# Kernel optimization log

Measured on AMD Instinct MI355X. Metric: run time of the kernel, lower is better.

The kernel has to match this reference:

```python
import jax, jax.numpy as jnp
import numpy as np

N = 50000
E = 800000
H = 128

def _mlp_params(key, sizes, biases):
    # sizes: list of (in, out); biases: list of bool
    params = []
    for i, ((fi, fo), b) in enumerate(zip(sizes, biases)):
        k = jax.random.fold_in(key, i)
        bound = 1.0 / np.sqrt(fi)
        W = jax.random.uniform(k, (fi, fo), minval=-bound, maxval=bound, dtype=jnp.float32)
        if b:
            bb = jax.random.uniform(jax.random.fold_in(k, 7), (fo,), minval=-bound, maxval=bound, dtype=jnp.float32)
        else:
            bb = None
        params.append((W, bb))
    return params

def setup_inputs() -> dict:
    key = jax.random.key(0)
    ks = jax.random.split(key, 8)
    h = jax.random.normal(ks[0], (N, H), dtype=jnp.float32)
    pos = jax.random.normal(ks[1], (N, 3), dtype=jnp.float32)
    edge_index = jax.random.randint(ks[2], (2, E), 0, N, dtype=jnp.int32)
    edge_p = _mlp_params(ks[3], [(2 * H + 1, H), (H, H)], [True, True])
    node_p = _mlp_params(ks[4], [(2 * H, H), (H, H)], [True, True])
    coord_p = _mlp_params(ks[5], [(H, H), (H, 1)], [True, False])
    return {
        'h': h, 'pos': pos, 'edge_index': edge_index,
        'eW0': edge_p[0][0], 'eb0': edge_p[0][1], 'eW1': edge_p[1][0], 'eb1': edge_p[1][1],
        'nW0': node_p[0][0], 'nb0': node_p[0][1], 'nW1': node_p[1][0], 'nb1': node_p[1][1],
        'cW0': coord_p[0][0], 'cb0': coord_p[0][1], 'cW1': coord_p[1][0],
    }

def reference(h, pos, edge_index, eW0, eb0, eW1, eb1, nW0, nb0, nW1, nb1, cW0, cb0, cW1):
    row, col = edge_index[0], edge_index[1]
    coord_diff = pos[row] - pos[col]                         # [E, 3]
    radial = jnp.sum(coord_diff ** 2, axis=1, keepdims=True)  # [E, 1]
    edge_feat = jnp.concatenate([h[row], h[col], radial], axis=1)  # [E, 2H+1]
    # edge MLP: Linear -> SiLU -> Linear -> SiLU
    m_ij = jax.nn.silu(edge_feat @ eW0 + eb0)
    m_ij = jax.nn.silu(m_ij @ eW1 + eb1)                     # [E, H]
    # coord MLP: Linear -> SiLU -> Linear(no bias)
    coord_weight = jax.nn.silu(m_ij @ cW0 + cb0) @ cW1       # [E, 1]
    norm = jnp.sqrt(radial + 1e-8)
    coord_update = coord_diff / norm * coord_weight          # [E, 3]
    # scatter-add messages to target nodes
    m_i = jax.ops.segment_sum(m_ij, row, num_segments=h.shape[0])
    node_in = jnp.concatenate([h, m_i], axis=1)              # [N, 2H]
    h_new = h + jax.nn.silu(node_in @ nW0 + nb0) @ nW1 + nb1
    pos_update = jax.ops.segment_sum(coord_update, row, num_segments=pos.shape[0])
    deg = jax.ops.segment_sum(jnp.ones((row.shape[0],), jnp.float32), row, num_segments=pos.shape[0])
    pos_new = pos + pos_update / (deg[:, None] + 1e-6)
    return h_new, pos_new
```

## Files before the change

### kernel.cpp

```cpp
#include <hip/hip_runtime.h>
#include <hip/hip_bf16.h>
#include <cstddef>

#define N_NODES 50000
#define N_EDGES 800000
#define HDIM    128
#define TME     64
#define TMN     64

#define RB128   272
#define RB256   528

#define SCHUNK  512
#define SNBLK   ((N_NODES + SCHUNK - 1) / SCHUNK)

typedef __attribute__((ext_vector_type(4))) float f32x4;
typedef __attribute__((ext_vector_type(8))) short bf16x8;

#define OFF_EW0T 0
#define OFF_EW0B 16384
#define OFF_EW1  32768
#define OFF_CW0  49152
#define OFF_NW0  65536
#define OFF_NW1  98304
#define PACK_ELEMS 114688

__device__ __forceinline__ float silu(float x) {
    float e = __expf(-x);
    return __fdividef(x, 1.0f + e);
}
__device__ __forceinline__ unsigned short f2bf(float f) {
    union { __hip_bfloat16 h; unsigned short u; } cv;
    cv.h = __float2bfloat16(f);
    return cv.u;
}
__device__ __forceinline__ unsigned int f2bf2(float a, float b) {
    union { __hip_bfloat162 h; unsigned int u; } cv;
    cv.h = __float22bfloat162_rn(float2{a, b});
    return cv.u;
}
__device__ __forceinline__ float bf2f(unsigned short u) {
    return __uint_as_float(((unsigned int)u) << 16);
}
__device__ __forceinline__ float bflo(unsigned int u) {
    return __uint_as_float(u << 16);
}
__device__ __forceinline__ float bfhi(unsigned int u) {
    return __uint_as_float(u & 0xffff0000u);
}

__global__ void pack_weights(const float* __restrict__ eW0, const float* __restrict__ eW1,
                             const float* __restrict__ cW0, const float* __restrict__ nW0,
                             const float* __restrict__ nW1, unsigned short* __restrict__ pack)
{
    int g = blockIdx.x * blockDim.x + threadIdx.x;
    int f = g >> 6;
    int lane = g & 63;
    const float* W; int base; int rowoff = 0;
    if (f < 32)       { W = eW0; base = OFF_EW0T; }
    else if (f < 64)  { W = eW0; base = OFF_EW0B; f -= 32; rowoff = 128; }
    else if (f < 96)  { W = eW1; base = OFF_EW1;  f -= 64; }
    else if (f < 128) { W = cW0; base = OFF_CW0;  f -= 96; }
    else if (f < 192) { W = nW0; base = OFF_NW0;  f -= 128; }
    else              { W = nW1; base = OFF_NW1;  f -= 192; }
    int KS = (base == OFF_NW0) ? 8 : 4;
    int cb = f / KS, ks = f % KS;
    int col = cb * 16 + (lane & 15);
    int kbase = rowoff + ks * 32 + ((lane >> 4) << 3);
#pragma unroll
    for (int j = 0; j < 8; ++j)
        pack[(size_t)base + ((size_t)(f * 64 + lane) * 8 + j)] =
            f2bf(W[(size_t)(kbase + j) * HDIM + col]);
}

__global__ __launch_bounds__(256)
void scanA_kernel(const int* __restrict__ cnt, int* __restrict__ bsum) {
    __shared__ int part[256];
    const int b = blockIdx.x, t = threadIdx.x;
    int i0 = b * SCHUNK + t * 2;
    int s = 0;
    if (i0 < N_NODES)     s += cnt[i0];
    if (i0 + 1 < N_NODES) s += cnt[i0 + 1];
    part[t] = s;
    __syncthreads();
    for (int off = 128; off > 0; off >>= 1) {
        if (t < off) part[t] += part[t + off];
        __syncthreads();
    }
    if (t == 0) bsum[b] = part[0];
}

__global__ __launch_bounds__(128)
void scanB_kernel(const int* __restrict__ bsum, int* __restrict__ boff,
                  int* __restrict__ row_start) {
    __shared__ int part[128];
    const int t = threadIdx.x;
    int s = (t < SNBLK) ? bsum[t] : 0;
    part[t] = s;
    __syncthreads();
    for (int off = 1; off < 128; off <<= 1) {
        int tmp = (t >= off) ? part[t - off] : 0;
        __syncthreads();
        part[t] += tmp;
        __syncthreads();
    }
    boff[t] = part[t] - s;
    if (t == 127) row_start[N_NODES] = part[127];
}

__global__ __launch_bounds__(256)
void scanC_kernel(const int* __restrict__ cnt, const int* __restrict__ boff,
                  int* __restrict__ row_start, int* __restrict__ cursor) {
    __shared__ int part[256];
    const int b = blockIdx.x, t = threadIdx.x;
    int i0 = b * SCHUNK + t * 2;
    int c0 = (i0 < N_NODES) ? cnt[i0] : 0;
    int c1 = (i0 + 1 < N_NODES) ? cnt[i0 + 1] : 0;
    int s = c0 + c1;
    part[t] = s;
    __syncthreads();
    for (int off = 1; off < 256; off <<= 1) {
        int tmp = (t >= off) ? part[t - off] : 0;
        __syncthreads();
        part[t] += tmp;
        __syncthreads();
    }
    int base = boff[b] + part[t] - s;
    if (i0 < N_NODES)     { row_start[i0] = base;          cursor[i0] = base; }
    if (i0 + 1 < N_NODES) { row_start[i0 + 1] = base + c0; cursor[i0 + 1] = base + c0; }
}

__global__ void scatter_kernel(const int* __restrict__ eidx, int* __restrict__ cursor,
                               int2* __restrict__ rc) {
    int e = (blockIdx.x * blockDim.x + threadIdx.x) * 4;
    if (e + 3 < N_EDGES) {
        int4 r4 = *(const int4*)(eidx + e);
        int4 c4 = *(const int4*)(eidx + N_EDGES + e);
        int p;
        p = atomicAdd(&cursor[r4.x], 1); rc[p] = int2{r4.x, c4.x};
        p = atomicAdd(&cursor[r4.y], 1); rc[p] = int2{r4.y, c4.y};
        p = atomicAdd(&cursor[r4.z], 1); rc[p] = int2{r4.z, c4.z};
        p = atomicAdd(&cursor[r4.w], 1); rc[p] = int2{r4.w, c4.w};
    } else {
        for (int i = e; i < N_EDGES; ++i) {
            int r = eidx[i], c = eidx[N_EDGES + i];
            int p = atomicAdd(&cursor[r], 1);
            rc[p] = int2{r, c};
        }
    }
}

template<int KS, int ROWB>
__device__ __forceinline__ void gemm_layer(const unsigned short* __restrict__ Bseg,
                                           const char* __restrict__ Xs,
                                           int lane, int cb, f32x4 acc[4])
{
    const bf16x8* bptr = (const bf16x8*)Bseg + (size_t)(cb * KS) * 64 + lane;
#pragma unroll
    for (int ks = 0; ks < KS; ++ks) {
        bf16x8 b = bptr[(size_t)ks * 64];
#pragma unroll
        for (int rb = 0; rb < 4; ++rb) {
            int row = rb * 16 + (lane & 15);
            bf16x8 a = *(const bf16x8*)(Xs + row * ROWB + ks * 64 + ((lane >> 4) << 4));
            acc[rb] = __builtin_amdgcn_mfma_f32_16x16x32_bf16(a, b, acc[rb], 0, 0, 0);
        }
    }
}

__global__ __launch_bounds__(512, 2)
void h0_kernel(const float* __restrict__ h, const float* __restrict__ eb0,
               const unsigned short* __restrict__ pack,
               const int* __restrict__ eidx, int* __restrict__ cnt,
               unsigned short* __restrict__ H0r, unsigned short* __restrict__ H0c)
{
    __shared__ __align__(16) char Xs[TMN * RB128];
    const int tid = threadIdx.x, lane = tid & 63, cb = tid >> 6;
    const int n0 = blockIdx.x * TMN;

    {
        int e = blockIdx.x * 1024 + tid * 2;
        if (e + 1 < N_EDGES) {
            int2 rr = *(const int2*)(eidx + e);
            atomicAdd(&cnt[rr.x], 1);
            atomicAdd(&cnt[rr.y], 1);
        } else if (e < N_EDGES) {
            atomicAdd(&cnt[eidx[e]], 1);
        }
    }

    {
        const int nl = tid >> 3, sub = tid & 7, n = n0 + nl;
        if (n < N_NODES) {
            const float4* h4 = (const float4*)(h + (size_t)n * HDIM);
#pragma unroll
            for (int q = 0; q < 4; ++q) {
                float4 f = h4[sub + q * 8];
                uint2 u; u.x = f2bf2(f.x, f.y); u.y = f2bf2(f.z, f.w);
                *(uint2*)(Xs + nl * RB128 + (sub + q * 8) * 8) = u;
            }
        } else {
            uint2 z{0, 0};
#pragma unroll
            for (int q = 0; q < 4; ++q)
                *(uint2*)(Xs + nl * RB128 + (sub + q * 8) * 8) = z;
        }
    }
    __syncthreads();

    const int col = cb * 16 + (lane & 15);
    f32x4 acc[4];
    {
        float bias = eb0[col];
#pragma unroll
        for (int rb = 0; rb < 4; ++rb) acc[rb] = f32x4{bias, bias, bias, bias};
        gemm_layer<4, RB128>(pack + OFF_EW0T, Xs, lane, cb, acc);
#pragma unroll
        for (int rb = 0; rb < 4; ++rb)
#pragma unroll
            for (int r = 0; r < 4; ++r) {
                int row = rb * 16 + ((lane >> 4) << 2) + r, n = n0 + row;
                if (n < N_NODES) H0r[(size_t)n * HDIM + col] = f2bf(acc[rb][r]);
            }
    }
    {
#pragma unroll
        for (int rb = 0; rb < 4; ++rb) acc[rb] = f32x4{0.f, 0.f, 0.f, 0.f};
        gemm_layer<4, RB128>(pack + OFF_EW0B, Xs, lane, cb, acc);
#pragma unroll
        for (int rb = 0; rb < 4; ++rb)
#pragma unroll
            for (int r = 0; r < 4; ++r) {
                int row = rb * 16 + ((lane >> 4) << 2) + r, n = n0 + row;
                if (n < N_NODES) H0c[(size_t)n * HDIM + col] = f2bf(acc[rb][r]);
            }
    }
}

__global__ __launch_bounds__(512, 4)
void egnn_edge_kernel(const unsigned short* __restrict__ H0r,
                      const unsigned short* __restrict__ H0c,
                      const float* __restrict__ pos,
                      const int2*  __restrict__ rc,
                      const float* __restrict__ w256,
                      const float* __restrict__ eb1, const float* __restrict__ cb0,
                      const float* __restrict__ cW1,
                      const unsigned short* __restrict__ pack,
                      float* __restrict__ m_i,
                      float* __restrict__ pos_upd)
{
    __shared__ __align__(16) char Ya[TME * RB128];
    __shared__ __align__(16) char Yb[TME * RB128];
    __shared__ float rad_s[TME];
    __shared__ float dif_s[TME][3];
    __shared__ float cu_s[TME][4];
    __shared__ int   rowb_s[TME];

    const int tid = threadIdx.x, lane = tid & 63, cb = tid >> 6;

    int lb;
    {
        const int nwg = gridDim.x;
        const int q = nwg >> 3, r = nwg & 7;
        const int xcd = blockIdx.x & 7, idx = blockIdx.x >> 3;
        lb = (xcd < r) ? (xcd * (q + 1) + idx) : (r * (q + 1) + (xcd - r) * q + idx);
    }
    const int e0 = lb * TME;

    {
        const int el = tid >> 3, sub = tid & 7, idx = e0 + el;
        const int2 rcv = rc[idx];
        const int r = rcv.x, c = rcv.y;
        float dx = pos[(size_t)r * 3 + 0] - pos[(size_t)c * 3 + 0];
        float dy = pos[(size_t)r * 3 + 1] - pos[(size_t)c * 3 + 1];
        float dz = pos[(size_t)r * 3 + 2] - pos[(size_t)c * 3 + 2];
        float rad = dx * dx + dy * dy + dz * dz;
        if (sub == 0) {
            rad_s[el] = rad;
            dif_s[el][0] = dx; dif_s[el][1] = dy; dif_s[el][2] = dz;
            rowb_s[el] = r;
        }
        const bf16x8* ar = (const bf16x8*)(H0r + (size_t)r * HDIM + sub * 16);
        const bf16x8* ac = (const bf16x8*)(H0c + (size_t)c * HDIM + sub * 16);
        bf16x8 a0 = ar[0], a1 = ar[1];
        bf16x8 c0 = ac[0], c1 = ac[1];
        const float4* wp = (const float4*)(w256 + sub * 16);
        float4 w4[4] = { wp[0], wp[1], wp[2], wp[3] };
        const float* wf = (const float*)w4;
        float v[16];
#pragma unroll
        for (int i = 0; i < 8; ++i) v[i]     = bf2f((unsigned short)a0[i]) + bf2f((unsigned short)c0[i]);
#pragma unroll
        for (int i = 0; i < 8; ++i) v[8 + i] = bf2f((unsigned short)a1[i]) + bf2f((unsigned short)c1[i]);
#pragma unroll
        for (int i = 0; i < 16; ++i) v[i] = silu(fmaf(rad, wf[i], v[i]));
#pragma unroll
        for (int c4 = 0; c4 < 4; ++c4) {
            uint2 u;
            u.x = f2bf2(v[c4 * 4 + 0], v[c4 * 4 + 1]);
            u.y = f2bf2(v[c4 * 4 + 2], v[c4 * 4 + 3]);
            *(uint2*)(Ya + el * RB128 + sub * 32 + c4 * 8) = u;
        }
    }
    __syncthreads();

    const int col = cb * 16 + (lane & 15);
    f32x4 acc[4];

    {
        float bias = eb1[col];
#pragma unroll
        for (int rb = 0; rb < 4; ++rb) acc[rb] = f32x4{bias, bias, bias, bias};
        gemm_layer<4, RB128>(pack + OFF_EW1, Ya, lane, cb, acc);
#pragma unroll
        for (int rb = 0; rb < 4; ++rb)
#pragma unroll
            for (int r = 0; r < 4; ++r) {
                int row = rb * 16 + ((lane >> 4) << 2) + r;
                *(unsigned short*)(Yb + row * RB128 + col * 2) = f2bf(silu(acc[rb][r]));
            }
    }
    __syncthreads();

    {
        const int rcol = tid & 127;
        const int ch   = tid >> 7;
        float run = 0.f;
        int cur = rowb_s[ch * 16];
#pragma unroll
        for (int i = 0; i < 16; ++i) {
            int row = ch * 16 + i;
            int rr = rowb_s[row];
            if (rr != cur) {
                atomicAdd(&m_i[(size_t)cur * HDIM + rcol], run);
                run = 0.f; cur = rr;
            }
            unsigned short u = *(const unsigned short*)(Yb + row * RB128 + rcol * 2);
            run += bf2f(u);
        }
        atomicAdd(&m_i[(size_t)cur * HDIM + rcol], run);
    }

    {
        float bias = cb0[col];
#pragma unroll
        for (int rb = 0; rb < 4; ++rb) acc[rb] = f32x4{bias, bias, bias, bias};
        gemm_layer<4, RB128>(pack + OFF_CW0, Yb, lane, cb, acc);
#pragma unroll
        for (int rb = 0; rb < 4; ++rb)
#pragma unroll
            for (int r = 0; r < 4; ++r) {
                int row = rb * 16 + ((lane >> 4) << 2) + r;
                *(unsigned short*)(Ya + row * RB128 + col * 2) = f2bf(silu(acc[rb][r]));
            }
    }
    __syncthreads();

    {
        const int el = tid >> 3, sub = tid & 7;
        float p = 0.f;
#pragma unroll
        for (int i = 0; i < 16; i += 2) {
            int jj = sub * 16 + i;
            unsigned int u = *(const unsigned int*)(Ya + el * RB128 + jj * 2);
            p = fmaf(bflo(u), cW1[jj], p);
            p = fmaf(bfhi(u), cW1[jj + 1], p);
        }
        p += __shfl_down(p, 4, 8);
        p += __shfl_down(p, 2, 8);
        p += __shfl_down(p, 1, 8);
        if (sub == 0) {
            float inv = 1.0f / sqrtf(rad_s[el] + 1e-8f);
            float cwv = p * inv;
            cu_s[el][0] = dif_s[el][0] * cwv;
            cu_s[el][1] = dif_s[el][1] * cwv;
            cu_s[el][2] = dif_s[el][2] * cwv;
        }
    }
    __syncthreads();

    if (tid < TME) {
        const int el = tid;
        bool head = (el == 0) || (rowb_s[el] != rowb_s[el - 1]);
        if (head) {
            float sx = 0.f, sy = 0.f, sz = 0.f;
            int r = rowb_s[el];
            int j = el;
            do {
                sx += cu_s[j][0]; sy += cu_s[j][1]; sz += cu_s[j][2];
                ++j;
            } while (j < TME && rowb_s[j] == r);
            atomicAdd(&pos_upd[(size_t)r * 3 + 0], sx);
            atomicAdd(&pos_upd[(size_t)r * 3 + 1], sy);
            atomicAdd(&pos_upd[(size_t)r * 3 + 2], sz);
        }
    }
}

__global__ __launch_bounds__(512)
void egnn_node_kernel(const float* __restrict__ h,
                      const float* __restrict__ pos,
                      const float* __restrict__ m_i,
                      const float* __restrict__ pos_upd,
                      const int*   __restrict__ row_start,
                      const float* __restrict__ nb0, const float* __restrict__ nb1,
                      const unsigned short* __restrict__ pack,
                      float* __restrict__ out_h,
                      float* __restrict__ out_pos)
{
    __shared__ __align__(16) char Xs[TMN * RB256];
    __shared__ __align__(16) char Ya[TMN * RB128];

    const int tid = threadIdx.x, lane = tid & 63, cb = tid >> 6;
    const int n0 = blockIdx.x * TMN;

    if (tid < TMN * 3) {
        int nl = tid / 3, d = tid % 3;
        int n = n0 + nl;
        if (n < N_NODES) {
            float dv = (float)(row_start[n + 1] - row_start[n]);
            out_pos[(size_t)n * 3 + d] =
                pos[(size_t)n * 3 + d] + pos_upd[(size_t)n * 3 + d] / (dv + 1e-6f);
        }
    }

    {
        const int nl = tid >> 3, sub = tid & 7, n = n0 + nl;
        if (n < N_NODES) {
            const float4* h4 = (const float4*)(h   + (size_t)n * HDIM);
            const float4* m4 = (const float4*)(m_i + (size_t)n * HDIM);
#pragma unroll
            for (int q = 0; q < 4; ++q) {
                float4 fh = h4[sub + q * 8];
                float4 fm = m4[sub + q * 8];
                uint2 uh; uh.x = f2bf2(fh.x, fh.y); uh.y = f2bf2(fh.z, fh.w);
                uint2 um; um.x = f2bf2(fm.x, fm.y); um.y = f2bf2(fm.z, fm.w);
                *(uint2*)(Xs + nl * RB256 + (sub + q * 8) * 8)       = uh;
                *(uint2*)(Xs + nl * RB256 + 256 + (sub + q * 8) * 8) = um;
            }
        } else {
            uint2 z{0, 0};
#pragma unroll
            for (int q = 0; q < 4; ++q) {
                *(uint2*)(Xs + nl * RB256 + (sub + q * 8) * 8)       = z;
                *(uint2*)(Xs + nl * RB256 + 256 + (sub + q * 8) * 8) = z;
            }
        }
    }
    __syncthreads();

    const int col = cb * 16 + (lane & 15);
    f32x4 acc[4];

    {
        float bias = nb0[col];
#pragma unroll
        for (int rb = 0; rb < 4; ++rb) acc[rb] = f32x4{bias, bias, bias, bias};
        gemm_layer<8, RB256>(pack + OFF_NW0, Xs, lane, cb, acc);
#pragma unroll
        for (int rb = 0; rb < 4; ++rb)
#pragma unroll
            for (int r = 0; r < 4; ++r) {
                int row = rb * 16 + ((lane >> 4) << 2) + r;
                *(unsigned short*)(Ya + row * RB128 + col * 2) = f2bf(silu(acc[rb][r]));
            }
    }
    __syncthreads();

    {
        float bias = nb1[col];
#pragma unroll
        for (int rb = 0; rb < 4; ++rb) acc[rb] = f32x4{bias, bias, bias, bias};
        gemm_layer<4, RB128>(pack + OFF_NW1, Ya, lane, cb, acc);
#pragma unroll
        for (int rb = 0; rb < 4; ++rb)
#pragma unroll
            for (int r = 0; r < 4; ++r) {
                int row = rb * 16 + ((lane >> 4) << 2) + r, n = n0 + row;
                if (n < N_NODES)
                    out_h[(size_t)n * HDIM + col] = h[(size_t)n * HDIM + col] + acc[rb][r];
            }
    }
}

extern "C" void kernel_launch(void* const* d_in, const int* in_sizes, int n_in,
                              void* d_out, int out_size, void* d_ws, size_t ws_size,
                              hipStream_t stream) {
    const float* h    = (const float*)d_in[0];
    const float* pos  = (const float*)d_in[1];
    const int*   eidx = (const int*)  d_in[2];
    const float* eW0  = (const float*)d_in[3];
    const float* eb0  = (const float*)d_in[4];
    const float* eW1  = (const float*)d_in[5];
    const float* eb1  = (const float*)d_in[6];
    const float* nW0  = (const float*)d_in[7];
    const float* nb0  = (const float*)d_in[8];
    const float* nW1  = (const float*)d_in[9];
    const float* nb1  = (const float*)d_in[10];
    const float* cW0  = (const float*)d_in[11];
    const float* cb0  = (const float*)d_in[12];
    const float* cW1  = (const float*)d_in[13];

    float* out_h   = (float*)d_out;
    float* out_pos = out_h + (size_t)N_NODES * HDIM;

    float* m_i       = (float*)d_ws;
    float* pos_upd   = m_i + (size_t)N_NODES * HDIM;
    int*   cnt       = (int*)(pos_upd + (size_t)N_NODES * 3);
    int*   row_start = cnt + N_NODES;
    int*   cursor    = row_start + N_NODES + 1;
    int*   bsum      = cursor + N_NODES;
    int*   boff      = bsum + 128;
    int2*  rc        = (int2*)(boff + 128);
    unsigned short* pack = (unsigned short*)(rc + N_EDGES);
    unsigned short* H0r  = pack + PACK_ELEMS;
    unsigned short* H0c  = H0r + (size_t)N_NODES * HDIM;

    size_t zero_bytes = ((size_t)N_NODES * HDIM + (size_t)N_NODES * 3 + N_NODES) * sizeof(float);
    hipMemsetAsync(m_i, 0, zero_bytes, stream);

    pack_weights<<<56, 256, 0, stream>>>(eW0, eW1, cW0, nW0, nW1, pack);

    h0_kernel<<<(N_NODES + TMN - 1) / TMN, 512, 0, stream>>>(h, eb0, pack, eidx, cnt, H0r, H0c);

    scanA_kernel<<<SNBLK, 256, 0, stream>>>(cnt, bsum);
    scanB_kernel<<<1, 128, 0, stream>>>(bsum, boff, row_start);
    scanC_kernel<<<SNBLK, 256, 0, stream>>>(cnt, boff, row_start, cursor);
    scatter_kernel<<<(N_EDGES / 4 + 255) / 256, 256, 0, stream>>>(eidx, cursor, rc);

    egnn_edge_kernel<<<N_EDGES / TME, 512, 0, stream>>>(
        H0r, H0c, pos, rc, eW0 + (size_t)256 * HDIM, eb1, cb0, cW1,
        pack, m_i, pos_upd);

    egnn_node_kernel<<<(N_NODES + TMN - 1) / TMN, 512, 0, stream>>>(
        h, pos, m_i, pos_upd, row_start, nb0, nb1, pack, out_h, out_pos);
}
```

Baseline: 356.0 us.

## Swap MFMA operands so accumulators hold contiguous features per row

The GEMM helper now passes the weights as the MFMA A operand and the activations as B, so each lane's accumulator holds four consecutive output features for a single row. All epilogues then write packed 4-wide bf16 or float4 values instead of scalar 2-byte stores, and bias loads become float4. The coord MLP's final dot product is fused into the register epilogue through cross-lane shuffles and a small per-wave partial buffer, which removes one LDS round trip and a block barrier. The correctness of this depends on the packed weight layout matching the transposed operand role.

Result: faster. 338.5 us (-4.9%).

```diff
diff --git a/kernel.cpp b/kernel.cpp
--- a/kernel.cpp
+++ b/kernel.cpp
@@ -151,19 +151,19 @@
 }
 
 template<int KS, int ROWB>
-__device__ __forceinline__ void gemm_layer(const unsigned short* __restrict__ Bseg,
-                                           const char* __restrict__ Xs,
-                                           int lane, int cb, f32x4 acc[4])
+__device__ __forceinline__ void gemm_layer_T(const unsigned short* __restrict__ Wseg,
+                                             const char* __restrict__ Xs,
+                                             int lane, int cb, f32x4 acc[4])
 {
-    const bf16x8* bptr = (const bf16x8*)Bseg + (size_t)(cb * KS) * 64 + lane;
+    const bf16x8* aptr = (const bf16x8*)Wseg + (size_t)(cb * KS) * 64 + lane;
 #pragma unroll
     for (int ks = 0; ks < KS; ++ks) {
-        bf16x8 b = bptr[(size_t)ks * 64];
-#pragma unroll
-        for (int rb = 0; rb < 4; ++rb) {
-            int row = rb * 16 + (lane & 15);
-            bf16x8 a = *(const bf16x8*)(Xs + row * ROWB + ks * 64 + ((lane >> 4) << 4));
-            acc[rb] = __builtin_amdgcn_mfma_f32_16x16x32_bf16(a, b, acc[rb], 0, 0, 0);
+        bf16x8 a = aptr[(size_t)ks * 64];
+#pragma unroll
+        for (int eb = 0; eb < 4; ++eb) {
+            int row = eb * 16 + (lane & 15);
+            bf16x8 b = *(const bf16x8*)(Xs + row * ROWB + ks * 64 + ((lane >> 4) << 4));
+            acc[eb] = __builtin_amdgcn_mfma_f32_16x16x32_bf16(a, b, acc[eb], 0, 0, 0);
         }
     }
 }
@@ -208,32 +208,34 @@
     }
     __syncthreads();
 
-    const int col = cb * 16 + (lane & 15);
+    const int j0 = cb * 16 + ((lane >> 4) << 2);
     f32x4 acc[4];
     {
-        float bias = eb0[col];
-#pragma unroll
-        for (int rb = 0; rb < 4; ++rb) acc[rb] = f32x4{bias, bias, bias, bias};
-        gemm_layer<4, RB128>(pack + OFF_EW0T, Xs, lane, cb, acc);
-#pragma unroll
-        for (int rb = 0; rb < 4; ++rb)
-#pragma unroll
-            for (int r = 0; r < 4; ++r) {
-                int row = rb * 16 + ((lane >> 4) << 2) + r, n = n0 + row;
-                if (n < N_NODES) H0r[(size_t)n * HDIM + col] = f2bf(acc[rb][r]);
-            }
-    }
-    {
-#pragma unroll
-        for (int rb = 0; rb < 4; ++rb) acc[rb] = f32x4{0.f, 0.f, 0.f, 0.f};
-        gemm_layer<4, RB128>(pack + OFF_EW0B, Xs, lane, cb, acc);
-#pragma unroll
-        for (int rb = 0; rb < 4; ++rb)
-#pragma unroll
-            for (int r = 0; r < 4; ++r) {
-                int row = rb * 16 + ((lane >> 4) << 2) + r, n = n0 + row;
-                if (n < N_NODES) H0c[(size_t)n * HDIM + col] = f2bf(acc[rb][r]);
-            }
+        float4 b0 = *(const float4*)(eb0 + j0);
+#pragma unroll
+        for (int eb = 0; eb < 4; ++eb) acc[eb] = f32x4{b0.x, b0.y, b0.z, b0.w};
+        gemm_layer_T<4, RB128>(pack + OFF_EW0T, Xs, lane, cb, acc);
+#pragma unroll
+        for (int eb = 0; eb < 4; ++eb) {
+            int n = n0 + eb * 16 + (lane & 15);
+            if (n < N_NODES) {
+                uint2 u; u.x = f2bf2(acc[eb][0], acc[eb][1]); u.y = f2bf2(acc[eb][2], acc[eb][3]);
+                *(uint2*)(H0r + (size_t)n * HDIM + j0) = u;
+            }
+        }
+    }
+    {
+#pragma unroll
+        for (int eb = 0; eb < 4; ++eb) acc[eb] = f32x4{0.f, 0.f, 0.f, 0.f};
+        gemm_layer_T<4, RB128>(pack + OFF_EW0B, Xs, lane, cb, acc);
+#pragma unroll
+        for (int eb = 0; eb < 4; ++eb) {
+            int n = n0 + eb * 16 + (lane & 15);
+            if (n < N_NODES) {
+                uint2 u; u.x = f2bf2(acc[eb][0], acc[eb][1]); u.y = f2bf2(acc[eb][2], acc[eb][3]);
+                *(uint2*)(H0c + (size_t)n * HDIM + j0) = u;
+            }
+        }
     }
 }
 
@@ -251,6 +253,7 @@
 {
     __shared__ __align__(16) char Ya[TME * RB128];
     __shared__ __align__(16) char Yb[TME * RB128];
+    __shared__ float pw[8][TME];
     __shared__ float rad_s[TME];
     __shared__ float dif_s[TME][3];
     __shared__ float cu_s[TME][4];
@@ -304,21 +307,22 @@
     }
     __syncthreads();
 
-    const int col = cb * 16 + (lane & 15);
+    const int j0 = cb * 16 + ((lane >> 4) << 2);
     f32x4 acc[4];
 
     {
-        float bias = eb1[col];
-#pragma unroll
-        for (int rb = 0; rb < 4; ++rb) acc[rb] = f32x4{bias, bias, bias, bias};
-        gemm_layer<4, RB128>(pack + OFF_EW1, Ya, lane, cb, acc);
-#pragma unroll
-        for (int rb = 0; rb < 4; ++rb)
-#pragma unroll
-            for (int r = 0; r < 4; ++r) {
-                int row = rb * 16 + ((lane >> 4) << 2) + r;
-                *(unsigned short*)(Yb + row * RB128 + col * 2) = f2bf(silu(acc[rb][r]));
-            }
+        float4 b1 = *(const float4*)(eb1 + j0);
+#pragma unroll
+        for (int eb = 0; eb < 4; ++eb) acc[eb] = f32x4{b1.x, b1.y, b1.z, b1.w};
+        gemm_layer_T<4, RB128>(pack + OFF_EW1, Ya, lane, cb, acc);
+#pragma unroll
+        for (int eb = 0; eb < 4; ++eb) {
+            int e = eb * 16 + (lane & 15);
+            float s0 = silu(acc[eb][0]), s1 = silu(acc[eb][1]);
+            float s2 = silu(acc[eb][2]), s3 = silu(acc[eb][3]);
+            uint2 u; u.x = f2bf2(s0, s1); u.y = f2bf2(s2, s3);
+            *(uint2*)(Yb + e * RB128 + j0 * 2) = u;
+        }
     }
     __syncthreads();
 
@@ -342,40 +346,39 @@
     }
 
     {
-        float bias = cb0[col];
-#pragma unroll
-        for (int rb = 0; rb < 4; ++rb) acc[rb] = f32x4{bias, bias, bias, bias};
-        gemm_layer<4, RB128>(pack + OFF_CW0, Yb, lane, cb, acc);
-#pragma unroll
-        for (int rb = 0; rb < 4; ++rb)
-#pragma unroll
-            for (int r = 0; r < 4; ++r) {
-                int row = rb * 16 + ((lane >> 4) << 2) + r;
-                *(unsigned short*)(Ya + row * RB128 + col * 2) = f2bf(silu(acc[rb][r]));
-            }
-    }
-    __syncthreads();
-
-    {
-        const int el = tid >> 3, sub = tid & 7;
-        float p = 0.f;
-#pragma unroll
-        for (int i = 0; i < 16; i += 2) {
-            int jj = sub * 16 + i;
-            unsigned int u = *(const unsigned int*)(Ya + el * RB128 + jj * 2);
-            p = fmaf(bflo(u), cW1[jj], p);
-            p = fmaf(bfhi(u), cW1[jj + 1], p);
-        }
-        p += __shfl_down(p, 4, 8);
-        p += __shfl_down(p, 2, 8);
-        p += __shfl_down(p, 1, 8);
-        if (sub == 0) {
-            float inv = 1.0f / sqrtf(rad_s[el] + 1e-8f);
-            float cwv = p * inv;
-            cu_s[el][0] = dif_s[el][0] * cwv;
-            cu_s[el][1] = dif_s[el][1] * cwv;
-            cu_s[el][2] = dif_s[el][2] * cwv;
-        }
+        float4 b2 = *(const float4*)(cb0 + j0);
+#pragma unroll
+        for (int eb = 0; eb < 4; ++eb) acc[eb] = f32x4{b2.x, b2.y, b2.z, b2.w};
+        gemm_layer_T<4, RB128>(pack + OFF_CW0, Yb, lane, cb, acc);
+        float4 w1 = *(const float4*)(cW1 + j0);
+        float pe[4];
+#pragma unroll
+        for (int eb = 0; eb < 4; ++eb) {
+            float p;
+            p = silu(acc[eb][0]) * w1.x;
+            p = fmaf(silu(acc[eb][1]), w1.y, p);
+            p = fmaf(silu(acc[eb][2]), w1.z, p);
+            p = fmaf(silu(acc[eb][3]), w1.w, p);
+            p += __shfl_xor(p, 16);
+            p += __shfl_xor(p, 32);
+            pe[eb] = p;
+        }
+        if (lane < 16) {
+#pragma unroll
+            for (int eb = 0; eb < 4; ++eb) pw[cb][eb * 16 + lane] = pe[eb];
+        }
+    }
+    __syncthreads();
+
+    if (tid < TME) {
+        float s = 0.f;
+#pragma unroll
+        for (int w = 0; w < 8; ++w) s += pw[w][tid];
+        float inv = 1.0f / sqrtf(rad_s[tid] + 1e-8f);
+        float cwv = s * inv;
+        cu_s[tid][0] = dif_s[tid][0] * cwv;
+        cu_s[tid][1] = dif_s[tid][1] * cwv;
+        cu_s[tid][2] = dif_s[tid][2] * cwv;
     }
     __syncthreads();
 
@@ -449,37 +452,41 @@
     }
     __syncthreads();
 
-    const int col = cb * 16 + (lane & 15);
+    const int j0 = cb * 16 + ((lane >> 4) << 2);
     f32x4 acc[4];
 
     {
-        float bias = nb0[col];
-#pragma unroll
-        for (int rb = 0; rb < 4; ++rb) acc[rb] = f32x4{bias, bias, bias, bias};
-        gemm_layer<8, RB256>(pack + OFF_NW0, Xs, lane, cb, acc);
-#pragma unroll
-        for (int rb = 0; rb < 4; ++rb)
-#pragma unroll
-            for (int r = 0; r < 4; ++r) {
-                int row = rb * 16 + ((lane >> 4) << 2) + r;
-                *(unsigned short*)(Ya + row * RB128 + col * 2) = f2bf(silu(acc[rb][r]));
-            }
-    }
-    __syncthreads();
-
-    {
-        float bias = nb1[col];
-#pragma unroll
-        for (int rb = 0; rb < 4; ++rb) acc[rb] = f32x4{bias, bias, bias, bias};
-        gemm_layer<4, RB128>(pack + OFF_NW1, Ya, lane, cb, acc);
-#pragma unroll
-        for (int rb = 0; rb < 4; ++rb)
-#pragma unroll
-            for (int r = 0; r < 4; ++r) {
-                int row = rb * 16 + ((lane >> 4) << 2) + r, n = n0 + row;
-                if (n < N_NODES)
-                    out_h[(size_t)n * HDIM + col] = h[(size_t)n * HDIM + col] + acc[rb][r];
-            }
+        float4 b0 = *(const float4*)(nb0 + j0);
+#pragma unroll
+        for (int eb = 0; eb < 4; ++eb) acc[eb] = f32x4{b0.x, b0.y, b0.z, b0.w};
+        gemm_layer_T<8, RB256>(pack + OFF_NW0, Xs, lane, cb, acc);
+#pragma unroll
+        for (int eb = 0; eb < 4; ++eb) {
+            int nl = eb * 16 + (lane & 15);
+            float s0 = silu(acc[eb][0]), s1 = silu(acc[eb][1]);
+            float s2 = silu(acc[eb][2]), s3 = silu(acc[eb][3]);
+            uint2 u; u.x = f2bf2(s0, s1); u.y = f2bf2(s2, s3);
+            *(uint2*)(Ya + nl * RB128 + j0 * 2) = u;
+        }
+    }
+    __syncthreads();
+
+    {
+        float4 b1 = *(const float4*)(nb1 + j0);
+#pragma unroll
+        for (int eb = 0; eb < 4; ++eb) acc[eb] = f32x4{b1.x, b1.y, b1.z, b1.w};
+        gemm_layer_T<4, RB128>(pack + OFF_NW1, Ya, lane, cb, acc);
+#pragma unroll
+        for (int eb = 0; eb < 4; ++eb) {
+            int n = n0 + eb * 16 + (lane & 15);
+            if (n < N_NODES) {
+                float4 hv = *(const float4*)(h + (size_t)n * HDIM + j0);
+                float4 o;
+                o.x = hv.x + acc[eb][0]; o.y = hv.y + acc[eb][1];
+                o.z = hv.z + acc[eb][2]; o.w = hv.w + acc[eb][3];
+                *(float4*)(out_h + (size_t)n * HDIM + j0) = o;
+            }
+        }
     }
 }
 
```
